# Optimization experiments

Measured on AMD Instinct MI355X. Metric: run time of the kernel, lower is better.

Reference implementation:

```python
import jax, jax.numpy as jnp
import numpy as np

B, S, L, H, D, FF, V = 2, 1024, 12, 12, 768, 3072, 50265
DH = D // H
W1 = 256                      # one-sided window (attention_window=512)
MOTIF = (31 + 96 + 80) * 2    # 414
MAXPOS = 4098
EPS = 1e-5
NEG = jnp.float32(-1e9)


def _ln(x, s, b):
    m = jnp.mean(x, -1, keepdims=True)
    v = jnp.mean(jnp.square(x - m), -1, keepdims=True)
    return (x - m) * jax.lax.rsqrt(v + EPS) * s + b


def setup_inputs() -> dict:
    key = jax.random.key(0)
    ks = iter(jax.random.split(key, 48))
    n = lambda *sh: jax.random.normal(next(ks), sh, jnp.float32) * 0.02
    return {
        "input_ids": jax.random.randint(next(ks), (B, S), 0, V),
        "attention_mask": jnp.ones((B, S), jnp.int32),
        "motif_dist": jax.random.uniform(next(ks), (B, MOTIF), dtype=jnp.float32),
        "emb_word": n(V, D), "emb_pos": n(MAXPOS, D), "emb_type": n(1, D),
        "emb_ln_s": jnp.ones((D,)), "emb_ln_b": jnp.zeros((D,)),
        "Wq": n(L, D, D), "bq": jnp.zeros((L, D)),
        "Wk": n(L, D, D), "bk": jnp.zeros((L, D)),
        "Wv": n(L, D, D), "bv": jnp.zeros((L, D)),
        "Wqg": n(L, D, D), "bqg": jnp.zeros((L, D)),
        "Wkg": n(L, D, D), "bkg": jnp.zeros((L, D)),
        "Wvg": n(L, D, D), "bvg": jnp.zeros((L, D)),
        "Wo": n(L, D, D), "bo": jnp.zeros((L, D)),
        "ln1_s": jnp.ones((L, D)), "ln1_b": jnp.zeros((L, D)),
        "Wi": n(L, D, FF), "bi": jnp.zeros((L, FF)),
        "Wo2": n(L, FF, D), "bo2": jnp.zeros((L, D)),
        "ln2_s": jnp.ones((L, D)), "ln2_b": jnp.zeros((L, D)),
        "head_Wd": n(D + MOTIF, D), "head_bd": jnp.zeros((D,)),
        "head_Wp": n(D, 2), "head_bp": jnp.zeros((2,)),
    }


def reference(input_ids, attention_mask, motif_dist, emb_word, emb_pos, emb_type,
              emb_ln_s, emb_ln_b, Wq, bq, Wk, bk, Wv, bv, Wqg, bqg, Wkg, bkg,
              Wvg, bvg, Wo, bo, ln1_s, ln1_b, Wi, bi, Wo2, bo2, ln2_s, ln2_b,
              head_Wd, head_bd, head_Wp, head_bp):
    Bn, Sn = input_ids.shape
    scale = 1.0 / np.sqrt(DH)
    # RoBERTa-style embeddings: positions start at padding_idx+1 = 2
    pos_ids = jnp.arange(Sn) + 2
    x = emb_word[input_ids] + emb_pos[pos_ids][None] + emb_type[0][None, None]
    x = _ln(x, emb_ln_s, emb_ln_b)

    key_valid = attention_mask.astype(bool)[:, None, None, :]      # [B,1,1,S]
    idx = jnp.arange(Sn)
    is_global = idx == 0                                           # default: CLS-only global
    band = jnp.abs(idx[:, None] - idx[None, :]) <= W1
    # local query attends to its sliding window plus all global keys
    local_allowed = (band | is_global[None, :])[None, None] & key_valid

    def heads(t, s):
        return t.reshape(Bn, s, H, DH).transpose(0, 2, 1, 3)       # [B,H,s,DH]

    for l in range(L):
        q = heads(x @ Wq[l] + bq[l], Sn) * scale
        k = heads(x @ Wk[l] + bk[l], Sn)
        v = heads(x @ Wv[l] + bv[l], Sn)
        scores = jnp.einsum('bhid,bhjd->bhij', q, k)
        probs = jax.nn.softmax(jnp.where(local_allowed, scores, NEG), -1)
        out = jnp.einsum('bhij,bhjd->bhid', probs, v)              # [B,H,S,DH]
        # global (CLS) query: full attention using the *_global projections
        qg = heads(x[:, :1] @ Wqg[l] + bqg[l], 1) * scale          # [B,H,1,DH]
        kg = heads(x @ Wkg[l] + bkg[l], Sn)
        vg = heads(x @ Wvg[l] + bvg[l], Sn)
        sg = jnp.einsum('bhid,bhjd->bhij', qg, kg)                 # [B,H,1,S]
        pg = jax.nn.softmax(jnp.where(key_valid, sg, NEG), -1)
        og = jnp.einsum('bhij,bhjd->bhid', pg, vg)                 # [B,H,1,DH]
        out = jnp.concatenate([og, out[:, :, 1:]], axis=2)
        out = out.transpose(0, 2, 1, 3).reshape(Bn, Sn, D)
        x = _ln(x + out @ Wo[l] + bo[l], ln1_s[l], ln1_b[l])
        h = jax.nn.gelu(x @ Wi[l] + bi[l], approximate=False)
        x = _ln(x + h @ Wo2[l] + bo2[l], ln2_s[l], ln2_b[l])

    # classification head: CLS hidden state concat motif distribution
    hcat = jnp.concatenate([x[:, 0, :], motif_dist], axis=-1)
    return jnp.tanh(hcat @ head_Wd + head_bd) @ head_Wp + head_bp
```

## Files before the change

### kernel.cpp

```cpp
#include <hip/hip_runtime.h>
#include <math.h>

typedef unsigned short u16;
typedef __attribute__((ext_vector_type(8))) short short8;
typedef __attribute__((ext_vector_type(4))) float f32x4;

#define BB 2
#define SS 1024
#define LL 12
#define HH 12
#define DD 768
#define FFF 3072
#define MOTIF 414
#define HCAT (DD + MOTIF)
#define W1 256
#define NEGV -1e9f
#define EPS 1e-5f
#define SCALE 0.125f
#define LD5 3840
#define WL_ELE 8257536

__device__ __forceinline__ float bf2f(u16 u) {
    union { unsigned i; float f; } x; x.i = ((unsigned)u) << 16; return x.f;
}
__device__ __forceinline__ u16 f2bf(float f) {
    union { float f; unsigned i; } x; x.f = f;
    unsigned r = x.i + 0x7fffu + ((x.i >> 16) & 1u);
    return (u16)(r >> 16);
}

__device__ __forceinline__ void gld16(const u16* g, u16* l) {
    __builtin_amdgcn_global_load_lds((const __attribute__((address_space(1))) void*)g,
                                     (__attribute__((address_space(3))) void*)l, 16, 0, 0);
}

__device__ __forceinline__ float block_reduce_sum(float v, float* red) {
    int t = threadIdx.x;
    red[t] = v; __syncthreads();
    #pragma unroll
    for (int s = 128; s > 0; s >>= 1) {
        if (t < s) red[t] += red[t + s];
        __syncthreads();
    }
    float r = red[0]; __syncthreads();
    return r;
}

__global__ __launch_bounds__(256) void embed_ln_kernel(
    const int* __restrict__ ids, const float* __restrict__ ew,
    const float* __restrict__ ep, const float* __restrict__ et,
    const float* __restrict__ gs, const float* __restrict__ gb,
    float* __restrict__ X, u16* __restrict__ Xb) {
    __shared__ float red[256];
    int row = blockIdx.x;
    int s = row % SS;
    int id = ids[row];
    int t = threadIdx.x;
    float v[3];
    float sum = 0.f;
    #pragma unroll
    for (int i = 0; i < 3; ++i) {
        int d = t + 256 * i;
        float x = ew[(size_t)id * DD + d] + ep[(size_t)(s + 2) * DD + d] + et[d];
        v[i] = x; sum += x;
    }
    sum = block_reduce_sum(sum, red);
    float m = sum * (1.f / DD);
    float sq = 0.f;
    #pragma unroll
    for (int i = 0; i < 3; ++i) { float c = v[i] - m; sq += c * c; }
    sq = block_reduce_sum(sq, red);
    float inv = rsqrtf(sq * (1.f / DD) + EPS);
    #pragma unroll
    for (int i = 0; i < 3; ++i) {
        int d = t + 256 * i;
        float o = (v[i] - m) * inv * gs[d] + gb[d];
        X[(size_t)row * DD + d] = o;
        Xb[(size_t)row * DD + d] = f2bf(o);
    }
}

__global__ __launch_bounds__(256) void add_ln_kernel(
    float* __restrict__ X, u16* __restrict__ Xb,
    const float* __restrict__ Tbase, int NT,
    const float* __restrict__ gs, const float* __restrict__ gb) {
    __shared__ float red[256];
    int row = blockIdx.x;
    int t = threadIdx.x;
    const size_t MN = (size_t)BB * SS * DD;
    float v[3];
    float sum = 0.f;
    #pragma unroll
    for (int i = 0; i < 3; ++i) {
        int d = t + 256 * i;
        size_t idx = (size_t)row * DD + d;
        float x = X[idx];
        for (int p = 0; p < NT; ++p) x += Tbase[p * MN + idx];
        v[i] = x; sum += x;
    }
    sum = block_reduce_sum(sum, red);
    float m = sum * (1.f / DD);
    float sq = 0.f;
    #pragma unroll
    for (int i = 0; i < 3; ++i) { float c = v[i] - m; sq += c * c; }
    sq = block_reduce_sum(sq, red);
    float inv = rsqrtf(sq * (1.f / DD) + EPS);
    #pragma unroll
    for (int i = 0; i < 3; ++i) {
        int d = t + 256 * i;
        float o = (v[i] - m) * inv * gs[d] + gb[d];
        X[(size_t)row * DD + d] = o;
        Xb[(size_t)row * DD + d] = f2bf(o);
    }
}

template <int LAYERED>
__global__ __launch_bounds__(256) void conv_all_kernel(
    const float* __restrict__ Wqp, const float* __restrict__ Wkp,
    const float* __restrict__ Wvp, const float* __restrict__ Wkgp,
    const float* __restrict__ Wvgp, const float* __restrict__ Wop,
    const float* __restrict__ Wip, const float* __restrict__ Wo2p,
    u16* __restrict__ WtBase) {
    __shared__ float Tt[64][65];
    int l = LAYERED ? blockIdx.y : 0;
    size_t oDD = (size_t)l * DD * DD;
    size_t oFF = (size_t)l * DD * FFF;
    u16* Wt6  = WtBase + (size_t)l * WL_ELE;
    u16* Wti  = Wt6 + 6 * DD * DD;
    u16* Wto2 = Wti + FFF * DD;
    int tid = blockIdx.x;
    const float* W; u16* Wt; int Nd, Kd, n0, k0;
    if (tid < 864) {
        int z = tid / 144, rem = tid % 144;
        const float* w6[6] = {Wqp + oDD, Wkp + oDD, Wvp + oDD, Wkgp + oDD, Wvgp + oDD, Wop + oDD};
        W = w6[z];
        Wt = Wt6 + (size_t)z * DD * DD;
        Nd = DD; Kd = DD; n0 = (rem % 12) * 64; k0 = (rem / 12) * 64;
    } else if (tid < 1440) {
        int i = tid - 864;
        W = Wip + oFF; Wt = Wti; Nd = FFF; Kd = DD; n0 = (i % 48) * 64; k0 = (i / 48) * 64;
    } else {
        int i = tid - 1440;
        W = Wo2p + oFF; Wt = Wto2; Nd = DD; Kd = FFF; n0 = (i % 12) * 64; k0 = (i / 12) * 64;
    }
    int t = threadIdx.x;
    {
        int rbase = t >> 4, c = (t & 15) * 4;
        #pragma unroll
        for (int i = 0; i < 4; ++i) {
            int r = rbase + i * 16;
            float4 v = *(const float4*)(W + (size_t)(k0 + r) * Nd + n0 + c);
            Tt[r][c + 0] = v.x; Tt[r][c + 1] = v.y;
            Tt[r][c + 2] = v.z; Tt[r][c + 3] = v.w;
        }
    }
    __syncthreads();
    {
        int nbase = t >> 3, kk = (t & 7) * 8;
        #pragma unroll
        for (int i = 0; i < 2; ++i) {
            int n = nbase + i * 32;
            union { uint4 v; u16 e[8]; } wv;
            #pragma unroll
            for (int j = 0; j < 8; ++j) wv.e[j] = f2bf(Tt[kk + j][n]);
            *(uint4*)&Wt[(size_t)(n0 + n) * Kd + k0 + kk] = wv.v;
        }
    }
}

__global__ __launch_bounds__(256) void bcat_kernel(
    const float* __restrict__ bq, const float* __restrict__ bk,
    const float* __restrict__ bv, const float* __restrict__ bkg,
    const float* __restrict__ bvg, float* __restrict__ bcat) {
    int tid = blockIdx.x * 256 + threadIdx.x;
    if (tid >= LL * LD5) return;
    int l = tid / LD5, r = tid % LD5, z = r / DD, j = r % DD;
    const float* src = (z == 0) ? bq : (z == 1) ? bk : (z == 2) ? bv : (z == 3) ? bkg : bvg;
    bcat[tid] = src[l * DD + j];
}

#define STAGE(j, buf)                                                                   \
    do {                                                                                \
        int _k0 = (j) << 5;                                                             \
        _Pragma("unroll")                                                               \
        for (int _op = 0; _op < 2; ++_op) {                                             \
            int _rc = rA + _op * 16;                                                    \
            int _r = _rc + rr;                                                          \
            gld16(A  + (size_t)(bm + _r) * K + kbeg + _k0 + ((s4 ^ (_r & 3)) * 8),      \
                  &As[buf][_rc * 32]);                                                  \
            gld16(Bt + (size_t)(bn + _r) * K + kbeg + _k0 + ((s4 ^ (_r & 3)) * 8),      \
                  &Bs[buf][_rc * 32]);                                                  \
        }                                                                               \
    } while (0)

template <int ACT, int OBF>
__global__ __launch_bounds__(256) void gemm_bf16(
    const u16* __restrict__ A, const u16* __restrict__ Bt,
    const float* __restrict__ bias, void* __restrict__ Cout,
    int M, int N, int K, int Ksplit) {
    __shared__ __align__(16) u16 As[2][128 * 32];
    __shared__ __align__(16) u16 Bs[2][128 * 32];
    int z = blockIdx.z;
    int kbeg = z * Ksplit;
    int kend = kbeg + Ksplit; if (kend > K) kend = K;
    int t = threadIdx.x, lane = t & 63, wv = t >> 6;
    int bm = blockIdx.y * 128, bn = blockIdx.x * 128;
    int wm = wv >> 1, wn = wv & 1;
    int h = lane >> 4, q15 = lane & 15;
    int rA = wv * 32;
    int rr = lane >> 2, s4 = lane & 3;
    f32x4 acc[4][4];
    #pragma unroll
    for (int i = 0; i < 4; ++i)
        #pragma unroll
        for (int j = 0; j < 4; ++j) { acc[i][j][0] = 0.f; acc[i][j][1] = 0.f; acc[i][j][2] = 0.f; acc[i][j][3] = 0.f; }

    int nk = (kend - kbeg) >> 5;
    STAGE(0, 0);
    if (nk > 1) STAGE(1, 1);
    int cur = 0;
    for (int i = 0; i < nk - 1; ++i) {
        asm volatile("s_waitcnt vmcnt(4)" ::: "memory");
        __builtin_amdgcn_s_barrier();
        short8 af[4], bfr[4];
        #pragma unroll
        for (int mf = 0; mf < 4; ++mf) {
            int row = wm * 64 + mf * 16 + q15;
            af[mf] = *(const short8*)&As[cur][row * 32 + ((h ^ (row & 3)) * 8)];
        }
        #pragma unroll
        for (int nf = 0; nf < 4; ++nf) {
            int row = wn * 64 + nf * 16 + q15;
            bfr[nf] = *(const short8*)&Bs[cur][row * 32 + ((h ^ (row & 3)) * 8)];
        }
        asm volatile("s_waitcnt lgkmcnt(0)" ::: "memory");
        __builtin_amdgcn_sched_barrier(0);
        __builtin_amdgcn_s_barrier();
        __builtin_amdgcn_sched_barrier(0);
        if (i + 2 < nk) STAGE(i + 2, cur);
        #pragma unroll
        for (int mf = 0; mf < 4; ++mf)
            #pragma unroll
            for (int nf = 0; nf < 4; ++nf)
                acc[mf][nf] = __builtin_amdgcn_mfma_f32_16x16x32_bf16(af[mf], bfr[nf], acc[mf][nf], 0, 0, 0);
        cur ^= 1;
    }
    asm volatile("s_waitcnt vmcnt(0)" ::: "memory");
    __builtin_amdgcn_s_barrier();
    {
        short8 af[4], bfr[4];
        #pragma unroll
        for (int mf = 0; mf < 4; ++mf) {
            int row = wm * 64 + mf * 16 + q15;
            af[mf] = *(const short8*)&As[cur][row * 32 + ((h ^ (row & 3)) * 8)];
        }
        #pragma unroll
        for (int nf = 0; nf < 4; ++nf) {
            int row = wn * 64 + nf * 16 + q15;
            bfr[nf] = *(const short8*)&Bs[cur][row * 32 + ((h ^ (row & 3)) * 8)];
        }
        #pragma unroll
        for (int mf = 0; mf < 4; ++mf)
            #pragma unroll
            for (int nf = 0; nf < 4; ++nf)
                acc[mf][nf] = __builtin_amdgcn_mfma_f32_16x16x32_bf16(af[mf], bfr[nf], acc[mf][nf], 0, 0, 0);
    }
    float* Cf = (float*)Cout + (size_t)z * M * N;
    u16*   Cb = (u16*)Cout;
    #pragma unroll
    for (int mf = 0; mf < 4; ++mf) {
        int mbase = bm + wm * 64 + mf * 16 + h * 4;
        #pragma unroll
        for (int nf = 0; nf < 4; ++nf) {
            int n = bn + wn * 64 + nf * 16 + q15;
            float bv = 0.f;
            if (z == 0) bv = bias[n];
            #pragma unroll
            for (int rg = 0; rg < 4; ++rg) {
                float val = acc[mf][nf][rg] + bv;
                if (ACT == 1) val = 0.5f * val * (1.f + erff(val * 0.70710678118654752f));
                if (OBF) Cb[(size_t)(mbase + rg) * N + n] = f2bf(val);
                else     Cf[(size_t)(mbase + rg) * N + n] = val;
            }
        }
    }
}

__global__ __launch_bounds__(256) void attn_local_mfma(
    const u16* __restrict__ QKV, const int* __restrict__ mask,
    u16* __restrict__ AO) {
    __shared__ __align__(16) u16 Qs[64 * 64];
    __shared__ __align__(16) u16 Ks[64 * 64];
    __shared__ __align__(16) u16 Vst[64 * 64];
    __shared__ __align__(16) u16 Pld[4][16 * 64];
    __shared__ float msk[64];
    int bid = blockIdx.x;
    int qt = bid & 15;
    int hh = (bid >> 4) % HH;
    int b  = bid / (16 * HH);
    int t = threadIdx.x, lane = t & 63, wv = t >> 6;
    int h = lane >> 4, q15 = lane & 15;
    int i0 = qt * 64;

    #pragma unroll
    for (int op = 0; op < 2; ++op) {
        int r = wv * 16 + op * 8 + (lane >> 3), s = lane & 7;
        gld16(QKV + (size_t)(b * SS + i0 + r) * LD5 + hh * 64 + ((s ^ (r & 7)) * 8),
              &Qs[(wv * 16 + op * 8) * 64]);
    }
    __syncthreads();
    short8 bq[2];
    {
        int qrow = wv * 16 + q15;
        #pragma unroll
        for (int ks = 0; ks < 2; ++ks)
            bq[ks] = *(const short8*)&Qs[qrow * 64 + (((ks * 4 + h) ^ (qrow & 7)) * 8)];
    }

    float mrun = -3e38f, lrun = 0.f;
    f32x4 o[4];
    #pragma unroll
    for (int nf = 0; nf < 4; ++nf) { o[nf][0] = 0.f; o[nf][1] = 0.f; o[nf][2] = 0.f; o[nf][3] = 0.f; }

    int jlo = i0 - W1; if (jlo < 0) jlo = 0;
    int jend = i0 + 64 + W1; if (jend > SS) jend = SS;
    int hasCLS = (jlo > 0) ? 1 : 0;
    int nt = hasCLS + (jend - jlo) / 64;
    int iq = i0 + wv * 16 + q15;

    for (int tt = 0; tt < nt; ++tt) {
        int base = (hasCLS && tt == 0) ? 0 : jlo + (tt - hasCLS) * 64;
        if (tt > 0) __syncthreads();
        #pragma unroll
        for (int op = 0; op < 2; ++op) {
            int r = wv * 16 + op * 8 + (lane >> 3), s = lane & 7;
            gld16(QKV + (size_t)(b * SS + base + r) * LD5 + 768 + hh * 64 + ((s ^ (r & 7)) * 8),
                  &Ks[(wv * 16 + op * 8) * 64]);
        }
        {
            int k2 = t & 31, dsec = t >> 5;
            const u16* vp = QKV + (size_t)(b * SS + base + 2 * k2) * LD5 + 1536 + hh * 64 + dsec * 8;
            union { uint4 v; u16 e[8]; } r0, r1;
            r0.v = *(const uint4*)vp;
            r1.v = *(const uint4*)(vp + LD5);
            int slot = k2 >> 2;
            #pragma unroll
            for (int j = 0; j < 8; ++j) {
                int d = dsec * 8 + j;
                unsigned val = (unsigned)r0.e[j] | ((unsigned)r1.e[j] << 16);
                *(unsigned*)&Vst[d * 64 + ((slot ^ (d & 7)) * 8) + ((2 * k2) & 7)] = val;
            }
        }
        if (t < 64) msk[t] = (float)mask[b * SS + base + t];
        __syncthreads();

        f32x4 sacc[4];
        #pragma unroll
        for (int kf = 0; kf < 4; ++kf) { sacc[kf][0] = 0.f; sacc[kf][1] = 0.f; sacc[kf][2] = 0.f; sacc[kf][3] = 0.f; }
        #pragma unroll
        for (int ks = 0; ks < 2; ++ks) {
            #pragma unroll
            for (int kf = 0; kf < 4; ++kf) {
                int krow = kf * 16 + q15;
                short8 afr = *(const short8*)&Ks[krow * 64 + (((ks * 4 + h) ^ (krow & 7)) * 8)];
                sacc[kf] = __builtin_amdgcn_mfma_f32_16x16x32_bf16(afr, bq[ks], sacc[kf], 0, 0, 0);
            }
        }
        float pv[4][4];
        float tmax = -3e38f;
        #pragma unroll
        for (int kf = 0; kf < 4; ++kf) {
            #pragma unroll
            for (int rg = 0; rg < 4; ++rg) {
                int kl = kf * 16 + h * 4 + rg;
                int key = base + kl;
                int dj = iq - key; int adj = dj < 0 ? -dj : dj;
                bool valid = ((adj <= W1) || (key == 0)) && (msk[kl] != 0.f);
                float s = valid ? sacc[kf][rg] * SCALE : NEGV;
                pv[kf][rg] = s;
                tmax = fmaxf(tmax, s);
            }
        }
        tmax = fmaxf(tmax, __shfl_xor(tmax, 16));
        tmax = fmaxf(tmax, __shfl_xor(tmax, 32));
        float mnew = fmaxf(mrun, tmax);
        float fac = __expf(mrun - mnew);
        mrun = mnew;
        float psum = 0.f;
        #pragma unroll
        for (int kf = 0; kf < 4; ++kf)
            #pragma unroll
            for (int rg = 0; rg < 4; ++rg) {
                float p = __expf(pv[kf][rg] - mnew);
                pv[kf][rg] = p; psum += p;
            }
        psum += __shfl_xor(psum, 16);
        psum += __shfl_xor(psum, 32);
        lrun = lrun * fac + psum;
        #pragma unroll
        for (int kf = 0; kf < 4; ++kf) {
            unsigned lo = (unsigned)f2bf(pv[kf][0]) | ((unsigned)f2bf(pv[kf][1]) << 16);
            unsigned hi = (unsigned)f2bf(pv[kf][2]) | ((unsigned)f2bf(pv[kf][3]) << 16);
            int slot = 2 * kf + (h >> 1);
            uint2 w; w.x = lo; w.y = hi;
            *(uint2*)&Pld[wv][q15 * 64 + ((slot ^ (q15 & 7)) * 8) + 4 * (h & 1)] = w;
        }
        float fo0 = __shfl(fac, (h * 4 + 0) | (lane & 48));
        float fo1 = __shfl(fac, (h * 4 + 1) | (lane & 48));
        float fo2 = __shfl(fac, (h * 4 + 2) | (lane & 48));
        float fo3 = __shfl(fac, (h * 4 + 3) | (lane & 48));
        #pragma unroll
        for (int nf = 0; nf < 4; ++nf) {
            o[nf][0] *= fo0; o[nf][1] *= fo1; o[nf][2] *= fo2; o[nf][3] *= fo3;
        }
        asm volatile("s_waitcnt lgkmcnt(0)" ::: "memory");
        #pragma unroll
        for (int ks = 0; ks < 2; ++ks) {
            short8 ap = *(const short8*)&Pld[wv][q15 * 64 + (((ks * 4 + h) ^ (q15 & 7)) * 8)];
            #pragma unroll
            for (int nf = 0; nf < 4; ++nf) {
                int d = nf * 16 + q15;
                short8 bvf = *(const short8*)&Vst[d * 64 + (((ks * 4 + h) ^ (d & 7)) * 8)];
                o[nf] = __builtin_amdgcn_mfma_f32_16x16x32_bf16(ap, bvf, o[nf], 0, 0, 0);
            }
        }
    }
    float linv = 1.f / lrun;
    float g0 = __shfl(linv, (h * 4 + 0) | (lane & 48));
    float g1 = __shfl(linv, (h * 4 + 1) | (lane & 48));
    float g2 = __shfl(linv, (h * 4 + 2) | (lane & 48));
    float g3 = __shfl(linv, (h * 4 + 3) | (lane & 48));
    size_t rb = (size_t)(b * SS + i0 + wv * 16 + h * 4);
    #pragma unroll
    for (int nf = 0; nf < 4; ++nf) {
        int d = hh * 64 + nf * 16 + q15;
        AO[(rb + 0) * DD + d] = f2bf(o[nf][0] * g0);
        AO[(rb + 1) * DD + d] = f2bf(o[nf][1] * g1);
        AO[(rb + 2) * DD + d] = f2bf(o[nf][2] * g2);
        AO[(rb + 3) * DD + d] = f2bf(o[nf][3] * g3);
    }
}

__global__ __launch_bounds__(512) void attn_global_kernel(
    const float* __restrict__ Xf, const float* __restrict__ Wqg,
    const float* __restrict__ bqg, const u16* __restrict__ QKV,
    const int* __restrict__ mask, u16* __restrict__ AO) {
    __shared__ float x0[DD];
    __shared__ float qv[64];
    __shared__ float sc[SS];
    __shared__ float red[512];
    __shared__ float part[8][64];
    int b = blockIdx.x / HH, hh = blockIdx.x % HH;
    int t = threadIdx.x;
    for (int i = t; i < DD; i += 512) x0[i] = Xf[(size_t)b * SS * DD + i];
    __syncthreads();
    {
        int d = t & 63, p = t >> 6;
        float acc = 0.f;
        int k0 = p * 96;
        #pragma unroll 8
        for (int k = k0; k < k0 + 96; ++k)
            acc += x0[k] * Wqg[(size_t)k * DD + hh * 64 + d];
        part[p][d] = acc;
    }
    __syncthreads();
    if (t < 64) {
        float s = bqg[hh * 64 + t];
        #pragma unroll
        for (int p = 0; p < 8; ++p) s += part[p][t];
        qv[t] = s * SCALE;
    }
    __syncthreads();
    for (int j = t; j < SS; j += 512) {
        const u16* kp = QKV + (size_t)(b * SS + j) * LD5 + 2304 + hh * 64;
        float acc = 0.f;
        #pragma unroll
        for (int d0 = 0; d0 < 64; d0 += 8) {
            union { uint4 v; u16 e[8]; } u;
            u.v = *(const uint4*)(kp + d0);
            #pragma unroll
            for (int j2 = 0; j2 < 8; ++j2) acc += qv[d0 + j2] * bf2f(u.e[j2]);
        }
        sc[j] = mask[b * SS + j] ? acc : NEGV;
    }
    __syncthreads();
    float mx = fmaxf(sc[t], sc[t + 512]);
    red[t] = mx; __syncthreads();
    #pragma unroll
    for (int s = 256; s > 0; s >>= 1) {
        if (t < s) red[t] = fmaxf(red[t], red[t + s]);
        __syncthreads();
    }
    mx = red[0]; __syncthreads();
    float e0 = __expf(sc[t] - mx), e1 = __expf(sc[t + 512] - mx);
    sc[t] = e0; sc[t + 512] = e1;
    red[t] = e0 + e1; __syncthreads();
    #pragma unroll
    for (int s = 256; s > 0; s >>= 1) {
        if (t < s) red[t] += red[t + s];
        __syncthreads();
    }
    float lsum = red[0]; __syncthreads();
    int g = t >> 6, d = t & 63;
    float acc = 0.f;
    for (int j = g; j < SS; j += 8)
        acc += sc[j] * bf2f(QKV[(size_t)(b * SS + j) * LD5 + 3072 + hh * 64 + d]);
    part[g][d] = acc;
    __syncthreads();
    if (g == 0) {
        float ov = 0.f;
        #pragma unroll
        for (int p = 0; p < 8; ++p) ov += part[p][d];
        AO[(size_t)(b * SS) * DD + hh * 64 + d] = f2bf(ov / lsum);
    }
}

__global__ __launch_bounds__(256) void head1_kernel(
    const float* __restrict__ X, const float* __restrict__ motif,
    const float* __restrict__ Wd, float* __restrict__ hpart) {
    __shared__ float hc[HCAT];
    __shared__ float part[4][64];
    int jb = blockIdx.x, kp = blockIdx.y, b = blockIdx.z;
    int t = threadIdx.x;
    for (int i = t; i < DD; i += 256) hc[i] = X[(size_t)b * SS * DD + i];
    for (int i = t; i < MOTIF; i += 256) hc[DD + i] = motif[(size_t)b * MOTIF + i];
    __syncthreads();
    int j = jb * 64 + (t & 63);
    int sub = t >> 6;
    int k0 = kp * 148 + sub * 37;
    int k1 = k0 + 37; if (k1 > HCAT) k1 = HCAT;
    float acc = 0.f;
    for (int k = k0; k < k1; ++k) acc += hc[k] * Wd[(size_t)k * DD + j];
    part[sub][t & 63] = acc;
    __syncthreads();
    if (sub == 0) {
        int x = t & 63;
        hpart[((size_t)b * 8 + kp) * DD + j] = part[0][x] + part[1][x] + part[2][x] + part[3][x];
    }
}

__global__ __launch_bounds__(256) void head2_kernel(
    const float* __restrict__ hpart, const float* __restrict__ bd,
    const float* __restrict__ Wp, const float* __restrict__ bp,
    float* __restrict__ out) {
    __shared__ float dvs[DD];
    __shared__ float red[256];
    int b = blockIdx.x;
    int t = threadIdx.x;
    for (int j = t; j < DD; j += 256) {
        float s = bd[j];
        #pragma unroll
        for (int kp = 0; kp < 8; ++kp) s += hpart[((size_t)b * 8 + kp) * DD + j];
        dvs[j] = tanhf(s);
    }
    __syncthreads();
    float a0 = 0.f, a1 = 0.f;
    for (int k = t; k < DD; k += 256) {
        a0 += dvs[k] * Wp[k * 2 + 0];
        a1 += dvs[k] * Wp[k * 2 + 1];
    }
    a0 = block_reduce_sum(a0, red);
    a1 = block_reduce_sum(a1, red);
    if (t == 0) {
        out[b * 2 + 0] = a0 + bp[0];
        out[b * 2 + 1] = a1 + bp[1];
    }
}

extern "C" void kernel_launch(void* const* d_in, const int* in_sizes, int n_in,
                              void* d_out, int out_size, void* d_ws, size_t ws_size,
                              hipStream_t stream) {
    const int*   input_ids = (const int*)d_in[0];
    const int*   attn_mask = (const int*)d_in[1];
    const float* motif     = (const float*)d_in[2];
    const float* emb_word  = (const float*)d_in[3];
    const float* emb_pos   = (const float*)d_in[4];
    const float* emb_type  = (const float*)d_in[5];
    const float* emb_ln_s  = (const float*)d_in[6];
    const float* emb_ln_b  = (const float*)d_in[7];
    const float* Wq  = (const float*)d_in[8];
    const float* bq  = (const float*)d_in[9];
    const float* Wk  = (const float*)d_in[10];
    const float* bk  = (const float*)d_in[11];
    const float* Wv  = (const float*)d_in[12];
    const float* bv  = (const float*)d_in[13];
    const float* Wqg = (const float*)d_in[14];
    const float* bqg = (const float*)d_in[15];
    const float* Wkg = (const float*)d_in[16];
    const float* bkg = (const float*)d_in[17];
    const float* Wvg = (const float*)d_in[18];
    const float* bvg = (const float*)d_in[19];
    const float* Wo  = (const float*)d_in[20];
    const float* bo  = (const float*)d_in[21];
    const float* ln1_s = (const float*)d_in[22];
    const float* ln1_b = (const float*)d_in[23];
    const float* Wi  = (const float*)d_in[24];
    const float* bi  = (const float*)d_in[25];
    const float* Wo2 = (const float*)d_in[26];
    const float* bo2 = (const float*)d_in[27];
    const float* ln2_s = (const float*)d_in[28];
    const float* ln2_b = (const float*)d_in[29];
    const float* head_Wd = (const float*)d_in[30];
    const float* head_bd = (const float*)d_in[31];
    const float* head_Wp = (const float*)d_in[32];
    const float* head_bp = (const float*)d_in[33];

    float* out = (float*)d_out;
    char* base = (char*)d_ws;

    float* Xf   = (float*)(base + 0);
    u16*   Xb   = (u16*)  (base + 6291456);
    u16*   QKVb = (u16*)  (base + 9437184);
    u16*   AOb  = (u16*)  (base + 25165824);
    float* T1f  = (float*)(base + 28311552);

    const size_t NEED_BIG  = 70225920;
    const size_t NEED_HUGE = 251891712;
    bool huge = ws_size >= NEED_HUGE;
    bool big  = huge || ws_size >= NEED_BIG;
    int NT = big ? 4 : 1;

    u16* WtAll; float* bcat; float* hpart;
    u16 *Wt6_s = nullptr, *Wti_s = nullptr, *Wto2_s = nullptr;
    if (huge) {
        bcat  = (float*)(base + 53477376);
        hpart = (float*)(base + 53661696);
        WtAll = (u16*)  (base + 53710848);
    } else {
        size_t wbase = big ? 53710848 : 34603008;
        Wt6_s  = (u16*)(base + wbase);
        Wti_s  = (u16*)(base + wbase + 7077888);
        Wto2_s = (u16*)(base + wbase + 11796480);
        bcat   = (float*)(base + wbase + 16515072);
        hpart  = (float*)(base + wbase + 16699392);
        WtAll  = Wt6_s;
    }
    u16* Hb = QKVb;

    const int nrow = BB * SS;

    embed_ln_kernel<<<nrow, 256, 0, stream>>>(input_ids, emb_word, emb_pos, emb_type,
                                              emb_ln_s, emb_ln_b, Xf, Xb);
    bcat_kernel<<<(LL * LD5 + 255) / 256, 256, 0, stream>>>(bq, bk, bv, bkg, bvg, bcat);
    if (huge)
        conv_all_kernel<1><<<dim3(2016, 12), 256, 0, stream>>>(
            Wq, Wk, Wv, Wkg, Wvg, Wo, Wi, Wo2, WtAll);

    dim3 g5(30, 16, 1);
    dim3 gO(6, 16, NT);
    dim3 gFF1(24, 16, 1);
    dim3 gFF2(6, 16, NT);

    for (int l = 0; l < LL; ++l) {
        size_t oDD = (size_t)l * DD * DD;
        u16 *Wt6, *Wti, *Wto2;
        if (huge) {
            Wt6  = WtAll + (size_t)l * WL_ELE;
            Wti  = Wt6 + 6 * DD * DD;
            Wto2 = Wti + FFF * DD;
        } else {
            conv_all_kernel<0><<<dim3(2016, 1), 256, 0, stream>>>(
                Wq + oDD, Wk + oDD, Wv + oDD, Wkg + oDD, Wvg + oDD, Wo + oDD,
                Wi + (size_t)l * DD * FFF, Wo2 + (size_t)l * FFF * DD, Wt6_s);
            Wt6 = Wt6_s; Wti = Wti_s; Wto2 = Wto2_s;
        }

        gemm_bf16<0, 1><<<g5, 256, 0, stream>>>(Xb, Wt6, bcat + l * LD5, QKVb,
                                                nrow, LD5, DD, DD);

        attn_local_mfma<<<BB * HH * 16, 256, 0, stream>>>(QKVb, attn_mask, AOb);
        attn_global_kernel<<<BB * HH, 512, 0, stream>>>(Xf, Wqg + oDD, bqg + l * DD,
                                                        QKVb, attn_mask, AOb);

        gemm_bf16<0, 0><<<gO, 256, 0, stream>>>(AOb, Wt6 + 5 * (size_t)DD * DD, bo + l * DD,
                                                T1f, nrow, DD, DD, DD / NT);
        add_ln_kernel<<<nrow, 256, 0, stream>>>(Xf, Xb, T1f, NT,
                                                ln1_s + l * DD, ln1_b + l * DD);

        gemm_bf16<1, 1><<<gFF1, 256, 0, stream>>>(Xb, Wti, bi + l * FFF, Hb,
                                                  nrow, FFF, DD, DD);
        gemm_bf16<0, 0><<<gFF2, 256, 0, stream>>>(Hb, Wto2, bo2 + l * DD,
                                                  T1f, nrow, DD, FFF, FFF / NT);
        add_ln_kernel<<<nrow, 256, 0, stream>>>(Xf, Xb, T1f, NT,
                                                ln2_s + l * DD, ln2_b + l * DD);
    }

    head1_kernel<<<dim3(12, 8, BB), 256, 0, stream>>>(Xf, motif, head_Wd, hpart);
    head2_kernel<<<BB, 256, 0, stream>>>(hpart, head_bd, head_Wp, head_bp, out);
}
```

Measured before the change: 2.400 ms.

## Fold global K/V projections into CLS query algebra, drop kg/vg GEMM columns

The global-key and global-value projections are removed from the fused QKV GEMM, which shrinks its output from 5 to 3 blocks of 768 columns. The CLS global attention kernel instead computes u = Wkg·q so that scores become x·u plus a bias term. It forms the output as (probs·X)·Wvg plus the bias in fp32 directly from the hidden states. This saves about 40% of the QKV GEMM work and the weight conversion, but the 24-block global kernel now streams the full fp32 X twice per head with scalar loops and may become a serial bottleneck.

```diff
diff --git a/kernel.cpp b/kernel.cpp
--- a/kernel.cpp
+++ b/kernel.cpp
@@ -17,8 +17,8 @@
 #define NEGV -1e9f
 #define EPS 1e-5f
 #define SCALE 0.125f
-#define LD5 3840
-#define WL_ELE 8257536
+#define LD3 2304
+#define WL_ELE 7077888
 
 __device__ __forceinline__ float bf2f(u16 u) {
     union { unsigned i; float f; } x; x.i = ((unsigned)u) << 16; return x.f;
@@ -117,30 +117,29 @@
 template <int LAYERED>
 __global__ __launch_bounds__(256) void conv_all_kernel(
     const float* __restrict__ Wqp, const float* __restrict__ Wkp,
-    const float* __restrict__ Wvp, const float* __restrict__ Wkgp,
-    const float* __restrict__ Wvgp, const float* __restrict__ Wop,
+    const float* __restrict__ Wvp, const float* __restrict__ Wop,
     const float* __restrict__ Wip, const float* __restrict__ Wo2p,
     u16* __restrict__ WtBase) {
     __shared__ float Tt[64][65];
     int l = LAYERED ? blockIdx.y : 0;
     size_t oDD = (size_t)l * DD * DD;
     size_t oFF = (size_t)l * DD * FFF;
-    u16* Wt6  = WtBase + (size_t)l * WL_ELE;
-    u16* Wti  = Wt6 + 6 * DD * DD;
+    u16* Wt4  = WtBase + (size_t)l * WL_ELE;
+    u16* Wti  = Wt4 + 4 * DD * DD;
     u16* Wto2 = Wti + FFF * DD;
     int tid = blockIdx.x;
     const float* W; u16* Wt; int Nd, Kd, n0, k0;
-    if (tid < 864) {
+    if (tid < 576) {
         int z = tid / 144, rem = tid % 144;
-        const float* w6[6] = {Wqp + oDD, Wkp + oDD, Wvp + oDD, Wkgp + oDD, Wvgp + oDD, Wop + oDD};
-        W = w6[z];
-        Wt = Wt6 + (size_t)z * DD * DD;
+        const float* w4[4] = {Wqp + oDD, Wkp + oDD, Wvp + oDD, Wop + oDD};
+        W = w4[z];
+        Wt = Wt4 + (size_t)z * DD * DD;
         Nd = DD; Kd = DD; n0 = (rem % 12) * 64; k0 = (rem / 12) * 64;
-    } else if (tid < 1440) {
-        int i = tid - 864;
+    } else if (tid < 1152) {
+        int i = tid - 576;
         W = Wip + oFF; Wt = Wti; Nd = FFF; Kd = DD; n0 = (i % 48) * 64; k0 = (i / 48) * 64;
     } else {
-        int i = tid - 1440;
+        int i = tid - 1152;
         W = Wo2p + oFF; Wt = Wto2; Nd = DD; Kd = FFF; n0 = (i % 12) * 64; k0 = (i / 12) * 64;
     }
     int t = threadIdx.x;
@@ -170,12 +169,11 @@
 
 __global__ __launch_bounds__(256) void bcat_kernel(
     const float* __restrict__ bq, const float* __restrict__ bk,
-    const float* __restrict__ bv, const float* __restrict__ bkg,
-    const float* __restrict__ bvg, float* __restrict__ bcat) {
+    const float* __restrict__ bv, float* __restrict__ bcat) {
     int tid = blockIdx.x * 256 + threadIdx.x;
-    if (tid >= LL * LD5) return;
-    int l = tid / LD5, r = tid % LD5, z = r / DD, j = r % DD;
-    const float* src = (z == 0) ? bq : (z == 1) ? bk : (z == 2) ? bv : (z == 3) ? bkg : bvg;
+    if (tid >= LL * LD3) return;
+    int l = tid / LD3, r = tid % LD3, z = r / DD, j = r % DD;
+    const float* src = (z == 0) ? bq : (z == 1) ? bk : bv;
     bcat[tid] = src[l * DD + j];
 }
 
@@ -305,7 +303,7 @@
     #pragma unroll
     for (int op = 0; op < 2; ++op) {
         int r = wv * 16 + op * 8 + (lane >> 3), s = lane & 7;
-        gld16(QKV + (size_t)(b * SS + i0 + r) * LD5 + hh * 64 + ((s ^ (r & 7)) * 8),
+        gld16(QKV + (size_t)(b * SS + i0 + r) * LD3 + hh * 64 + ((s ^ (r & 7)) * 8),
               &Qs[(wv * 16 + op * 8) * 64]);
     }
     __syncthreads();
@@ -334,15 +332,15 @@
         #pragma unroll
         for (int op = 0; op < 2; ++op) {
             int r = wv * 16 + op * 8 + (lane >> 3), s = lane & 7;
-            gld16(QKV + (size_t)(b * SS + base + r) * LD5 + 768 + hh * 64 + ((s ^ (r & 7)) * 8),
+            gld16(QKV + (size_t)(b * SS + base + r) * LD3 + 768 + hh * 64 + ((s ^ (r & 7)) * 8),
                   &Ks[(wv * 16 + op * 8) * 64]);
         }
         {
             int k2 = t & 31, dsec = t >> 5;
-            const u16* vp = QKV + (size_t)(b * SS + base + 2 * k2) * LD5 + 1536 + hh * 64 + dsec * 8;
+            const u16* vp = QKV + (size_t)(b * SS + base + 2 * k2) * LD3 + 1536 + hh * 64 + dsec * 8;
             union { uint4 v; u16 e[8]; } r0, r1;
             r0.v = *(const uint4*)vp;
-            r1.v = *(const uint4*)(vp + LD5);
+            r1.v = *(const uint4*)(vp + LD3);
             int slot = k2 >> 2;
             #pragma unroll
             for (int j = 0; j < 8; ++j) {
@@ -443,16 +441,22 @@
 
 __global__ __launch_bounds__(512) void attn_global_kernel(
     const float* __restrict__ Xf, const float* __restrict__ Wqg,
-    const float* __restrict__ bqg, const u16* __restrict__ QKV,
-    const int* __restrict__ mask, u16* __restrict__ AO) {
+    const float* __restrict__ bqg, const float* __restrict__ Wkg,
+    const float* __restrict__ bkg, const float* __restrict__ Wvg,
+    const float* __restrict__ bvg, const int* __restrict__ mask,
+    u16* __restrict__ AO) {
     __shared__ float x0[DD];
     __shared__ float qv[64];
+    __shared__ float uu[DD];
+    __shared__ float wvec[DD];
     __shared__ float sc[SS];
     __shared__ float red[512];
     __shared__ float part[8][64];
+    __shared__ float cbias;
     int b = blockIdx.x / HH, hh = blockIdx.x % HH;
     int t = threadIdx.x;
-    for (int i = t; i < DD; i += 512) x0[i] = Xf[(size_t)b * SS * DD + i];
+    const float* Xrow = Xf + (size_t)b * SS * DD;
+    for (int i = t; i < DD; i += 512) x0[i] = Xrow[i];
     __syncthreads();
     {
         int d = t & 63, p = t >> 6;
@@ -471,17 +475,34 @@
         qv[t] = s * SCALE;
     }
     __syncthreads();
+    for (int k = t; k < DD; k += 512) {
+        const float* wr = Wkg + (size_t)k * DD + hh * 64;
+        float acc = 0.f;
+        #pragma unroll
+        for (int d = 0; d < 64; d += 4) {
+            float4 w4 = *(const float4*)(wr + d);
+            acc += w4.x * qv[d] + w4.y * qv[d + 1] + w4.z * qv[d + 2] + w4.w * qv[d + 3];
+        }
+        uu[k] = acc;
+    }
+    if (t < 64) part[0][t] = qv[t] * bkg[hh * 64 + t];
+    __syncthreads();
+    if (t == 0) {
+        float c = 0.f;
+        #pragma unroll
+        for (int d = 0; d < 64; ++d) c += part[0][d];
+        cbias = c;
+    }
+    __syncthreads();
     for (int j = t; j < SS; j += 512) {
-        const u16* kp = QKV + (size_t)(b * SS + j) * LD5 + 2304 + hh * 64;
+        const float* xr = Xrow + (size_t)j * DD;
         float acc = 0.f;
-        #pragma unroll
-        for (int d0 = 0; d0 < 64; d0 += 8) {
-            union { uint4 v; u16 e[8]; } u;
-            u.v = *(const uint4*)(kp + d0);
-            #pragma unroll
-            for (int j2 = 0; j2 < 8; ++j2) acc += qv[d0 + j2] * bf2f(u.e[j2]);
-        }
-        sc[j] = mask[b * SS + j] ? acc : NEGV;
+        #pragma unroll 4
+        for (int d = 0; d < DD; d += 4) {
+            float4 xv = *(const float4*)(xr + d);
+            acc += xv.x * uu[d] + xv.y * uu[d + 1] + xv.z * uu[d + 2] + xv.w * uu[d + 3];
+        }
+        sc[j] = mask[b * SS + j] ? (acc + cbias) : NEGV;
     }
     __syncthreads();
     float mx = fmaxf(sc[t], sc[t + 512]);
@@ -501,17 +522,29 @@
         __syncthreads();
     }
     float lsum = red[0]; __syncthreads();
-    int g = t >> 6, d = t & 63;
-    float acc = 0.f;
-    for (int j = g; j < SS; j += 8)
-        acc += sc[j] * bf2f(QKV[(size_t)(b * SS + j) * LD5 + 3072 + hh * 64 + d]);
-    part[g][d] = acc;
-    __syncthreads();
-    if (g == 0) {
-        float ov = 0.f;
-        #pragma unroll
-        for (int p = 0; p < 8; ++p) ov += part[p][d];
-        AO[(size_t)(b * SS) * DD + hh * 64 + d] = f2bf(ov / lsum);
+    for (int k = t; k < DD; k += 512) {
+        float acc = 0.f;
+        #pragma unroll 8
+        for (int j = 0; j < SS; ++j)
+            acc += sc[j] * Xrow[(size_t)j * DD + k];
+        wvec[k] = acc;
+    }
+    __syncthreads();
+    {
+        int d = t & 63, p = t >> 6;
+        float acc = 0.f;
+        int k0 = p * 96;
+        #pragma unroll 8
+        for (int k = k0; k < k0 + 96; ++k)
+            acc += wvec[k] * Wvg[(size_t)k * DD + hh * 64 + d];
+        part[p][d] = acc;
+    }
+    __syncthreads();
+    if (t < 64) {
+        float s = 0.f;
+        #pragma unroll
+        for (int p = 0; p < 8; ++p) s += part[p][t];
+        AO[(size_t)(b * SS) * DD + hh * 64 + t] = f2bf(s / lsum + bvg[hh * 64 + t]);
     }
 }
 
@@ -611,29 +644,29 @@
     float* Xf   = (float*)(base + 0);
     u16*   Xb   = (u16*)  (base + 6291456);
     u16*   QKVb = (u16*)  (base + 9437184);
-    u16*   AOb  = (u16*)  (base + 25165824);
-    float* T1f  = (float*)(base + 28311552);
-
-    const size_t NEED_BIG  = 70225920;
-    const size_t NEED_HUGE = 251891712;
+    u16*   AOb  = (u16*)  (base + 18874368);
+    float* T1f  = (float*)(base + 22020096);
+
+    const size_t NEED_BIG  = 61661184;
+    const size_t NEED_HUGE = 217214976;
     bool huge = ws_size >= NEED_HUGE;
     bool big  = huge || ws_size >= NEED_BIG;
     int NT = big ? 4 : 1;
 
     u16* WtAll; float* bcat; float* hpart;
-    u16 *Wt6_s = nullptr, *Wti_s = nullptr, *Wto2_s = nullptr;
+    u16 *Wt4_s = nullptr, *Wti_s = nullptr, *Wto2_s = nullptr;
     if (huge) {
-        bcat  = (float*)(base + 53477376);
-        hpart = (float*)(base + 53661696);
-        WtAll = (u16*)  (base + 53710848);
+        bcat  = (float*)(base + 47185920);
+        hpart = (float*)(base + 47296512);
+        WtAll = (u16*)  (base + 47345664);
     } else {
-        size_t wbase = big ? 53710848 : 34603008;
-        Wt6_s  = (u16*)(base + wbase);
-        Wti_s  = (u16*)(base + wbase + 7077888);
-        Wto2_s = (u16*)(base + wbase + 11796480);
-        bcat   = (float*)(base + wbase + 16515072);
-        hpart  = (float*)(base + wbase + 16699392);
-        WtAll  = Wt6_s;
+        size_t wbase = big ? 47345664 : 28311552;
+        Wt4_s  = (u16*)(base + wbase);
+        Wti_s  = (u16*)(base + wbase + 4718592);
+        Wto2_s = (u16*)(base + wbase + 9437184);
+        bcat   = (float*)(base + wbase + 14155776);
+        hpart  = (float*)(base + wbase + 14266368);
+        WtAll  = Wt4_s;
     }
     u16* Hb = QKVb;
 
@@ -641,38 +674,39 @@
 
     embed_ln_kernel<<<nrow, 256, 0, stream>>>(input_ids, emb_word, emb_pos, emb_type,
                                               emb_ln_s, emb_ln_b, Xf, Xb);
-    bcat_kernel<<<(LL * LD5 + 255) / 256, 256, 0, stream>>>(bq, bk, bv, bkg, bvg, bcat);
+    bcat_kernel<<<(LL * LD3 + 255) / 256, 256, 0, stream>>>(bq, bk, bv, bcat);
     if (huge)
-        conv_all_kernel<1><<<dim3(2016, 12), 256, 0, stream>>>(
-            Wq, Wk, Wv, Wkg, Wvg, Wo, Wi, Wo2, WtAll);
-
-    dim3 g5(30, 16, 1);
+        conv_all_kernel<1><<<dim3(1728, 12), 256, 0, stream>>>(
+            Wq, Wk, Wv, Wo, Wi, Wo2, WtAll);
+
+    dim3 g3(18, 16, 1);
     dim3 gO(6, 16, NT);
     dim3 gFF1(24, 16, 1);
     dim3 gFF2(6, 16, NT);
 
     for (int l = 0; l < LL; ++l) {
         size_t oDD = (size_t)l * DD * DD;
-        u16 *Wt6, *Wti, *Wto2;
+        u16 *Wt4, *Wti, *Wto2;
         if (huge) {
-            Wt6  = WtAll + (size_t)l * WL_ELE;
-            Wti  = Wt6 + 6 * DD * DD;
+            Wt4  = WtAll + (size_t)l * WL_ELE;
+            Wti  = Wt4 + 4 * DD * DD;
             Wto2 = Wti + FFF * DD;
         } else {
-            conv_all_kernel<0><<<dim3(2016, 1), 256, 0, stream>>>(
-                Wq + oDD, Wk + oDD, Wv + oDD, Wkg + oDD, Wvg + oDD, Wo + oDD,
-                Wi + (size_t)l * DD * FFF, Wo2 + (size_t)l * FFF * DD, Wt6_s);
-            Wt6 = Wt6_s; Wti = Wti_s; Wto2 = Wto2_s;
-        }
-
-        gemm_bf16<0, 1><<<g5, 256, 0, stream>>>(Xb, Wt6, bcat + l * LD5, QKVb,
-                                                nrow, LD5, DD, DD);
+            conv_all_kernel<0><<<dim3(1728, 1), 256, 0, stream>>>(
+                Wq + oDD, Wk + oDD, Wv + oDD, Wo + oDD,
+                Wi + (size_t)l * DD * FFF, Wo2 + (size_t)l * FFF * DD, Wt4_s);
+            Wt4 = Wt4_s; Wti = Wti_s; Wto2 = Wto2_s;
+        }
+
+        gemm_bf16<0, 1><<<g3, 256, 0, stream>>>(Xb, Wt4, bcat + l * LD3, QKVb,
+                                                nrow, LD3, DD, DD);
 
         attn_local_mfma<<<BB * HH * 16, 256, 0, stream>>>(QKVb, attn_mask, AOb);
-        attn_global_kernel<<<BB * HH, 512, 0, stream>>>(Xf, Wqg + oDD, bqg + l * DD,
-                                                        QKVb, attn_mask, AOb);
-
-        gemm_bf16<0, 0><<<gO, 256, 0, stream>>>(AOb, Wt6 + 5 * (size_t)DD * DD, bo + l * DD,
+        attn_global_kernel<<<BB * HH, 512, 0, stream>>>(
+            Xf, Wqg + oDD, bqg + l * DD, Wkg + oDD, bkg + l * DD,
+            Wvg + oDD, bvg + l * DD, attn_mask, AOb);
+
+        gemm_bf16<0, 0><<<gO, 256, 0, stream>>>(AOb, Wt4 + 3 * (size_t)DD * DD, bo + l * DD,
                                                 T1f, nrow, DD, DD, DD / NT);
         add_ln_kernel<<<nrow, 256, 0, stream>>>(Xf, Xb, T1f, NT,
                                                 ln1_s + l * DD, ln1_b + l * DD);
```

Measured after the change: 4.312 ms. +79.7%, slower.
